# Kernel optimization log

Hardware: AMD Instinct MI355X
Metric: run time of the kernel (lower is better)

Reference implementation:

```python
import jax, jax.numpy as jnp
import numpy as np

B, S, D = 4, 2048, 1024


def setup_inputs() -> dict:
    key = jax.random.key(0)
    ks = jax.random.split(key, 7)
    s = 1.0 / np.sqrt(D)
    return {
        "x": jax.random.normal(ks[0], (B, S, D), dtype=jnp.float32),
        "Wq": jax.random.normal(ks[1], (D, D), dtype=jnp.float32) * s,
        "bq": jax.random.normal(ks[2], (D,), dtype=jnp.float32) * s,
        "Wk": jax.random.normal(ks[3], (D, D), dtype=jnp.float32) * s,
        "bk": jax.random.normal(ks[4], (D,), dtype=jnp.float32) * s,
        "Wv": jax.random.normal(ks[5], (D, D), dtype=jnp.float32) * s,
        "bv": jax.random.normal(ks[6], (D,), dtype=jnp.float32) * s,
    }


def reference(x, Wq, bq, Wk, bk, Wv, bv):
    # Linear layers: y = x @ W^T + b (torch nn.Linear convention)
    Q = jnp.einsum("bsd,ed->bse", x, Wq) + bq  # [B,S,D]
    K = jnp.einsum("bsd,ed->bse", x, Wk) + bk
    V = jnp.einsum("bsd,ed->bse", x, Wv) + bv
    d = x.shape[-1]
    scores = jnp.einsum("bqd,bkd->bqk", Q, K) / jnp.sqrt(jnp.float32(d))  # [B,S,S]
    weights = jax.nn.softmax(scores, axis=-1)
    O = jnp.einsum("bqk,bkd->bqd", weights, V)  # [B,S,D]
    return O
```

## Files before the change

kernel.cpp:

```cpp
#include <hip/hip_runtime.h>

typedef __bf16    bf16x8 __attribute__((ext_vector_type(8)));
typedef __bf16    bf16x4 __attribute__((ext_vector_type(4)));
typedef float     f32x4  __attribute__((ext_vector_type(4)));

#define BM 128
#define BN 128
#define BK 64

__device__ __forceinline__ void gload_lds16(const __bf16* g, __bf16* l) {
  __builtin_amdgcn_global_load_lds(
      (const __attribute__((address_space(1))) void*)g,
      (__attribute__((address_space(3))) void*)l,
      16, 0, 0);
}

__global__ void cvt_all(const float* __restrict__ x, const float* __restrict__ Wq,
                        const float* __restrict__ Wk, const float* __restrict__ Wv,
                        __bf16* __restrict__ xb, __bf16* __restrict__ Wqk,
                        __bf16* __restrict__ Wvb, float* __restrict__ lsum) {
  int b = blockIdx.x;
  if (b == 0) {
    for (int j = threadIdx.x; j < 8192; j += 256) lsum[j] = 0.f;
  }
  const float* src;
  __bf16* dst;
  int i;
  if (b < 8192) {
    src = x; dst = xb; i = b * 256 + threadIdx.x;
  } else {
    b -= 8192;
    const int mat = b >> 10;
    i = (b & 1023) * 256 + threadIdx.x;
    src = (mat == 0) ? Wq : (mat == 1) ? Wk : Wv;
    dst = (mat == 0) ? Wqk : (mat == 1) ? (Wqk + 1048576) : Wvb;
  }
  float4 v = ((const float4*)src)[i];
  bf16x4 o;
  o[0] = (__bf16)v.x; o[1] = (__bf16)v.y; o[2] = (__bf16)v.z; o[3] = (__bf16)v.w;
  ((bf16x4*)dst)[i] = o;
}

__device__ __forceinline__ void gemm_core(
    const __bf16* __restrict__ A, const __bf16* __restrict__ B,
    int lda, int ldb, int K, int bm0, int bn0,
    int tid, int wm, int wn, int quad, int l15,
    __bf16* As, __bf16* Bs, f32x4 (&acc)[4][4])
{
  const __bf16* Ag[4];
  const __bf16* Bg[4];
#pragma unroll
  for (int c = 0; c < 4; ++c) {
    const int r  = c * 32 + (tid >> 3);
    const int g  = (tid & 7) ^ (r & 7);
    Ag[c] = A + (size_t)(bm0 + r) * lda + g * 8;
    Bg[c] = B + (size_t)(bn0 + r) * ldb + g * 8;
  }

  for (int k0 = 0; k0 < K; k0 += BK) {
#pragma unroll
    for (int c = 0; c < 4; ++c) {
      gload_lds16(Ag[c] + k0, &As[c * 2048 + tid * 8]);
      gload_lds16(Bg[c] + k0, &Bs[c * 2048 + tid * 8]);
    }
    __syncthreads();

#pragma unroll
    for (int kk = 0; kk < 2; ++kk) {
      bf16x8 af[4], bfv[4];
#pragma unroll
      for (int i = 0; i < 4; ++i) {
        const int R = wm + i * 16 + l15;
        af[i] = *(const bf16x8*)&As[R * BK + (((kk * 4 + quad) ^ (R & 7)) * 8)];
      }
#pragma unroll
      for (int i = 0; i < 4; ++i) {
        const int R = wn + i * 16 + l15;
        bfv[i] = *(const bf16x8*)&Bs[R * BK + (((kk * 4 + quad) ^ (R & 7)) * 8)];
      }
#pragma unroll
      for (int mi = 0; mi < 4; ++mi)
#pragma unroll
        for (int ni = 0; ni < 4; ++ni)
          acc[mi][ni] = __builtin_amdgcn_mfma_f32_16x16x32_bf16(
              af[mi], bfv[ni], acc[mi][ni], 0, 0, 0);
    }
    __syncthreads();
  }
}

__global__ __launch_bounds__(256, 2)
void proj_qkv(const __bf16* __restrict__ xb, const __bf16* __restrict__ Wqk,
              const __bf16* __restrict__ Wvb,
              const float* __restrict__ bq, const float* __restrict__ bk,
              const float* __restrict__ bv,
              __bf16* __restrict__ Q, __bf16* __restrict__ Kb,
              __bf16* __restrict__ Vt)
{
  const int bid  = blockIdx.x;
  const int tid  = threadIdx.x;
  const int wave = tid >> 6;
  const int lane = tid & 63;
  const int quad = lane >> 4;
  const int l15  = lane & 15;
  const int wm   = (wave >> 1) * 64;
  const int wn   = (wave & 1) * 64;

  const bool isQK = bid < 1024;
  const __bf16* A;
  const __bf16* B;
  int bm0, bn0;
  if (isQK) {
    A = xb;  B = Wqk;
    bm0 = (bid & 63) * BM;  bn0 = (bid >> 6) * BN;
  } else {
    const int b2 = bid - 1024;
    A = Wvb; B = xb;
    bm0 = (b2 & 7) * BM;    bn0 = (b2 >> 3) * BN;
  }

  __shared__ __align__(16) __bf16 As[BM * BK];
  __shared__ __align__(16) __bf16 Bs[BN * BK];

  f32x4 acc[4][4];
#pragma unroll
  for (int i = 0; i < 4; ++i)
#pragma unroll
    for (int j = 0; j < 4; ++j)
      acc[i][j] = (f32x4){0.f, 0.f, 0.f, 0.f};

  gemm_core(A, B, 1024, 1024, 1024, bm0, bn0, tid, wm, wn, quad, l15,
            As, Bs, acc);

  if (isQK) {
#pragma unroll
    for (int mi = 0; mi < 4; ++mi) {
#pragma unroll
      for (int ni = 0; ni < 4; ++ni) {
        const int gn  = bn0 + wn + ni * 16 + l15;
        const int mat = gn >> 10;
        const int d   = gn & 1023;
        const float* bias = (mat == 0) ? bq : bk;
        __bf16* dst = (mat == 0) ? Q : Kb;
        const float bvv = bias[d];
#pragma unroll
        for (int r = 0; r < 4; ++r) {
          const int gm = bm0 + wm + mi * 16 + quad * 4 + r;
          dst[(size_t)gm * 1024 + d] = (__bf16)(acc[mi][ni][r] + bvv);
        }
      }
    }
  } else {
#pragma unroll
    for (int mi = 0; mi < 4; ++mi) {
#pragma unroll
      for (int ni = 0; ni < 4; ++ni) {
        const int gn = bn0 + wn + ni * 16 + l15;
        const int b  = gn >> 11, s = gn & 2047;
#pragma unroll
        for (int r = 0; r < 4; ++r) {
          const int gm = bm0 + wm + mi * 16 + quad * 4 + r;
          Vt[(size_t)b * (1024 * 2048) + (size_t)gm * 2048 + s] =
              (__bf16)(acc[mi][ni][r] + bv[gm]);
        }
      }
    }
  }
}

template<int MODE>
__global__ __launch_bounds__(256, 2)
void gemm_bt(const __bf16* __restrict__ A, const __bf16* __restrict__ B,
             float* __restrict__ C,
             int lda, int ldb, int ldc, int K,
             long sA, long sB, long sC,
             float* __restrict__ lsum,
             __bf16* __restrict__ out0)
{
  A += (long)blockIdx.z * sA;
  B += (long)blockIdx.z * sB;

  const int tid  = threadIdx.x;
  const int wave = tid >> 6;
  const int lane = tid & 63;
  const int quad = lane >> 4;
  const int l15  = lane & 15;
  const int bm0  = blockIdx.x * BM;
  const int bn0  = blockIdx.y * BN;
  const int wm   = (wave >> 1) * 64;
  const int wn   = (wave & 1) * 64;

  __shared__ __align__(16) __bf16 As[BM * BK];
  __shared__ __align__(16) __bf16 Bs[BN * BK];

  f32x4 acc[4][4];
#pragma unroll
  for (int i = 0; i < 4; ++i)
#pragma unroll
    for (int j = 0; j < 4; ++j)
      acc[i][j] = (f32x4){0.f, 0.f, 0.f, 0.f};

  gemm_core(A, B, lda, ldb, K, bm0, bn0, tid, wm, wn, quad, l15,
            As, Bs, acc);

  if (MODE == 2) {
#pragma unroll
    for (int mi = 0; mi < 4; ++mi) {
#pragma unroll
      for (int r = 0; r < 4; ++r) {
        const int gm = bm0 + wm + mi * 16 + quad * 4 + r;
        float part = 0.f;
#pragma unroll
        for (int ni = 0; ni < 4; ++ni) {
          const int gn = bn0 + wn + ni * 16 + l15;
          const __bf16 eb = (__bf16)__expf(acc[mi][ni][r] * 0.03125f);
          out0[(long)blockIdx.z * sC + (size_t)gm * ldc + gn] = eb;
          part += (float)eb;
        }
        part += __shfl_xor(part, 1);
        part += __shfl_xor(part, 2);
        part += __shfl_xor(part, 4);
        part += __shfl_xor(part, 8);
        if (l15 == 0)
          atomicAdd(&lsum[blockIdx.z * 2048 + gm], part);
      }
    }
  } else {
#pragma unroll
    for (int mi = 0; mi < 4; ++mi) {
#pragma unroll
      for (int r = 0; r < 4; ++r) {
        const int gm = bm0 + wm + mi * 16 + quad * 4 + r;
        const float rv = 1.0f / lsum[blockIdx.z * 2048 + gm];
#pragma unroll
        for (int ni = 0; ni < 4; ++ni) {
          const int gn = bn0 + wn + ni * 16 + l15;
          C[(long)blockIdx.z * sC + (size_t)gm * ldc + gn] = acc[mi][ni][r] * rv;
        }
      }
    }
  }
}

extern "C" void kernel_launch(void* const* d_in, const int* in_sizes, int n_in,
                              void* d_out, int out_size, void* d_ws, size_t ws_size,
                              hipStream_t stream) {
  const float* x  = (const float*)d_in[0];
  const float* Wq = (const float*)d_in[1];
  const float* bq = (const float*)d_in[2];
  const float* Wk = (const float*)d_in[3];
  const float* bk = (const float*)d_in[4];
  const float* Wv = (const float*)d_in[5];
  const float* bv = (const float*)d_in[6];
  float* out = (float*)d_out;

  char* ws = (char*)d_ws;
  __bf16* Q    = (__bf16*)(ws);
  __bf16* Kb   = (__bf16*)(ws + (16ull << 20));
  __bf16* Vt   = (__bf16*)(ws + (32ull << 20));
  __bf16* xb   = (__bf16*)(ws + (48ull << 20));
  __bf16* Wqk  = (__bf16*)(ws + (64ull << 20));
  __bf16* Wvb  = (__bf16*)(ws + (68ull << 20));
  __bf16* Sc   = (__bf16*)(ws + (48ull << 20));
  float*  lsum = (float*)(ws + (110ull << 20));

  dim3 blk(256);

  cvt_all<<<11264, blk, 0, stream>>>(x, Wq, Wk, Wv, xb, Wqk, Wvb, lsum);

  proj_qkv<<<1536, blk, 0, stream>>>(xb, Wqk, Wvb, bq, bk, bv, Q, Kb, Vt);

  gemm_bt<2><<<dim3(16, 16, 4), blk, 0, stream>>>(
      Q, Kb, nullptr, 1024, 1024, 2048, 1024,
      2048L * 1024, 2048L * 1024, 2048L * 2048,
      lsum, Sc);

  gemm_bt<3><<<dim3(16, 8, 4), blk, 0, stream>>>(
      Sc, Vt, out, 2048, 2048, 1024, 2048,
      2048L * 2048, 1024L * 2048, 2048L * 1024,
      lsum, nullptr);
}
```

Baseline: 245.0 us.

## Fuse all attention stages into one persistent kernel with grid barriers

Replaces the four separate launches (convert, QKV projection, scores+exp, PV) with one persistent kernel of 512 blocks that loops over tiles and separates stages with atomic-counter grid barriers. lsum and the barrier counter are zeroed by a memset. This removes per-launch overhead and inter-kernel gaps. In exchange it depends on all 512 blocks being co-resident to avoid deadlock, and the persistent tile loops may balance load less evenly than a full grid would (for example 1536 projection tiles over 512 blocks).

```diff
diff --git a/kernel.cpp b/kernel.cpp
--- a/kernel.cpp
+++ b/kernel.cpp
@@ -7,6 +7,7 @@
 #define BM 128
 #define BN 128
 #define BK 64
+#define NBLK 512
 
 __device__ __forceinline__ void gload_lds16(const __bf16* g, __bf16* l) {
   __builtin_amdgcn_global_load_lds(
@@ -15,34 +16,20 @@
       16, 0, 0);
 }
 
-__global__ void cvt_all(const float* __restrict__ x, const float* __restrict__ Wq,
-                        const float* __restrict__ Wk, const float* __restrict__ Wv,
-                        __bf16* __restrict__ xb, __bf16* __restrict__ Wqk,
-                        __bf16* __restrict__ Wvb, float* __restrict__ lsum) {
-  int b = blockIdx.x;
-  if (b == 0) {
-    for (int j = threadIdx.x; j < 8192; j += 256) lsum[j] = 0.f;
-  }
-  const float* src;
-  __bf16* dst;
-  int i;
-  if (b < 8192) {
-    src = x; dst = xb; i = b * 256 + threadIdx.x;
-  } else {
-    b -= 8192;
-    const int mat = b >> 10;
-    i = (b & 1023) * 256 + threadIdx.x;
-    src = (mat == 0) ? Wq : (mat == 1) ? Wk : Wv;
-    dst = (mat == 0) ? Wqk : (mat == 1) ? (Wqk + 1048576) : Wvb;
-  }
-  float4 v = ((const float4*)src)[i];
-  bf16x4 o;
-  o[0] = (__bf16)v.x; o[1] = (__bf16)v.y; o[2] = (__bf16)v.z; o[3] = (__bf16)v.w;
-  ((bf16x4*)dst)[i] = o;
+__device__ __forceinline__ void grid_barrier(unsigned* bar, unsigned target) {
+  __syncthreads();
+  if (threadIdx.x == 0) {
+    __threadfence();
+    atomicAdd(bar, 1u);
+    while (atomicAdd(bar, 0u) < target)
+      __builtin_amdgcn_s_sleep(2);
+    __threadfence();
+  }
+  __syncthreads();
 }
 
 __device__ __forceinline__ void gemm_core(
-    const __bf16* __restrict__ A, const __bf16* __restrict__ B,
+    const __bf16* A, const __bf16* B,
     int lda, int ldb, int K, int bm0, int bn0,
     int tid, int wm, int wn, int quad, int l15,
     __bf16* As, __bf16* Bs, f32x4 (&acc)[4][4])
@@ -90,14 +77,14 @@
 }
 
 __global__ __launch_bounds__(256, 2)
-void proj_qkv(const __bf16* __restrict__ xb, const __bf16* __restrict__ Wqk,
-              const __bf16* __restrict__ Wvb,
-              const float* __restrict__ bq, const float* __restrict__ bk,
-              const float* __restrict__ bv,
-              __bf16* __restrict__ Q, __bf16* __restrict__ Kb,
-              __bf16* __restrict__ Vt)
+void fused_attn(const float* __restrict__ x,  const float* __restrict__ Wq,
+                const float* __restrict__ bq, const float* __restrict__ Wk,
+                const float* __restrict__ bk, const float* __restrict__ Wv,
+                const float* __restrict__ bv, float* out,
+                __bf16* Q, __bf16* Kb, __bf16* Vt,
+                __bf16* xb, __bf16* Wqk, __bf16* Wvb,
+                __bf16* Sc, float* lsum, unsigned* bar)
 {
-  const int bid  = blockIdx.x;
   const int tid  = threadIdx.x;
   const int wave = tid >> 6;
   const int lane = tid & 63;
@@ -106,104 +93,110 @@
   const int wm   = (wave >> 1) * 64;
   const int wn   = (wave & 1) * 64;
 
-  const bool isQK = bid < 1024;
-  const __bf16* A;
-  const __bf16* B;
-  int bm0, bn0;
-  if (isQK) {
-    A = xb;  B = Wqk;
-    bm0 = (bid & 63) * BM;  bn0 = (bid >> 6) * BN;
-  } else {
-    const int b2 = bid - 1024;
-    A = Wvb; B = xb;
-    bm0 = (b2 & 7) * BM;    bn0 = (b2 >> 3) * BN;
-  }
-
   __shared__ __align__(16) __bf16 As[BM * BK];
   __shared__ __align__(16) __bf16 Bs[BN * BK];
 
-  f32x4 acc[4][4];
-#pragma unroll
-  for (int i = 0; i < 4; ++i)
-#pragma unroll
-    for (int j = 0; j < 4; ++j)
-      acc[i][j] = (f32x4){0.f, 0.f, 0.f, 0.f};
-
-  gemm_core(A, B, 1024, 1024, 1024, bm0, bn0, tid, wm, wn, quad, l15,
-            As, Bs, acc);
-
-  if (isQK) {
-#pragma unroll
-    for (int mi = 0; mi < 4; ++mi) {
-#pragma unroll
-      for (int ni = 0; ni < 4; ++ni) {
-        const int gn  = bn0 + wn + ni * 16 + l15;
-        const int mat = gn >> 10;
-        const int d   = gn & 1023;
-        const float* bias = (mat == 0) ? bq : bk;
-        __bf16* dst = (mat == 0) ? Q : Kb;
-        const float bvv = bias[d];
-#pragma unroll
-        for (int r = 0; r < 4; ++r) {
-          const int gm = bm0 + wm + mi * 16 + quad * 4 + r;
-          dst[(size_t)gm * 1024 + d] = (__bf16)(acc[mi][ni][r] + bvv);
-        }
-      }
-    }
-  } else {
-#pragma unroll
-    for (int mi = 0; mi < 4; ++mi) {
-#pragma unroll
-      for (int ni = 0; ni < 4; ++ni) {
-        const int gn = bn0 + wn + ni * 16 + l15;
-        const int b  = gn >> 11, s = gn & 2047;
-#pragma unroll
-        for (int r = 0; r < 4; ++r) {
-          const int gm = bm0 + wm + mi * 16 + quad * 4 + r;
-          Vt[(size_t)b * (1024 * 2048) + (size_t)gm * 2048 + s] =
-              (__bf16)(acc[mi][ni][r] + bv[gm]);
-        }
-      }
-    }
-  }
-}
-
-template<int MODE>
-__global__ __launch_bounds__(256, 2)
-void gemm_bt(const __bf16* __restrict__ A, const __bf16* __restrict__ B,
-             float* __restrict__ C,
-             int lda, int ldb, int ldc, int K,
-             long sA, long sB, long sC,
-             float* __restrict__ lsum,
-             __bf16* __restrict__ out0)
-{
-  A += (long)blockIdx.z * sA;
-  B += (long)blockIdx.z * sB;
-
-  const int tid  = threadIdx.x;
-  const int wave = tid >> 6;
-  const int lane = tid & 63;
-  const int quad = lane >> 4;
-  const int l15  = lane & 15;
-  const int bm0  = blockIdx.x * BM;
-  const int bn0  = blockIdx.y * BN;
-  const int wm   = (wave >> 1) * 64;
-  const int wn   = (wave & 1) * 64;
-
-  __shared__ __align__(16) __bf16 As[BM * BK];
-  __shared__ __align__(16) __bf16 Bs[BN * BK];
-
-  f32x4 acc[4][4];
-#pragma unroll
-  for (int i = 0; i < 4; ++i)
-#pragma unroll
-    for (int j = 0; j < 4; ++j)
-      acc[i][j] = (f32x4){0.f, 0.f, 0.f, 0.f};
-
-  gemm_core(A, B, lda, ldb, K, bm0, bn0, tid, wm, wn, quad, l15,
-            As, Bs, acc);
-
-  if (MODE == 2) {
+  {
+    const int g = blockIdx.x * 256 + tid;
+    const int gs = NBLK * 256;
+    for (int i = g; i < 2097152; i += gs) {
+      float4 v = ((const float4*)x)[i];
+      bf16x4 o;
+      o[0] = (__bf16)v.x; o[1] = (__bf16)v.y; o[2] = (__bf16)v.z; o[3] = (__bf16)v.w;
+      ((bf16x4*)xb)[i] = o;
+    }
+    for (int i = g; i < 786432; i += gs) {
+      const int mat = i >> 18;
+      const int j   = i & 262143;
+      const float* src = (mat == 0) ? Wq : (mat == 1) ? Wk : Wv;
+      __bf16* dst = (mat == 0) ? Wqk : (mat == 1) ? (Wqk + 1048576) : Wvb;
+      float4 v = ((const float4*)src)[j];
+      bf16x4 o;
+      o[0] = (__bf16)v.x; o[1] = (__bf16)v.y; o[2] = (__bf16)v.z; o[3] = (__bf16)v.w;
+      ((bf16x4*)dst)[j] = o;
+    }
+  }
+  grid_barrier(bar, NBLK);
+
+  for (int t = blockIdx.x; t < 1536; t += NBLK) {
+    const bool isQK = t < 1024;
+    const __bf16* A;
+    const __bf16* B;
+    int bm0, bn0;
+    if (isQK) {
+      A = xb;  B = Wqk;
+      bm0 = (t & 63) * BM;  bn0 = (t >> 6) * BN;
+    } else {
+      const int b2 = t - 1024;
+      A = Wvb; B = xb;
+      bm0 = (b2 & 7) * BM;  bn0 = (b2 >> 3) * BN;
+    }
+
+    f32x4 acc[4][4];
+#pragma unroll
+    for (int i = 0; i < 4; ++i)
+#pragma unroll
+      for (int j = 0; j < 4; ++j)
+        acc[i][j] = (f32x4){0.f, 0.f, 0.f, 0.f};
+
+    gemm_core(A, B, 1024, 1024, 1024, bm0, bn0, tid, wm, wn, quad, l15,
+              As, Bs, acc);
+
+    if (isQK) {
+#pragma unroll
+      for (int mi = 0; mi < 4; ++mi) {
+#pragma unroll
+        for (int ni = 0; ni < 4; ++ni) {
+          const int gn  = bn0 + wn + ni * 16 + l15;
+          const int mat = gn >> 10;
+          const int d   = gn & 1023;
+          const float* bias = (mat == 0) ? bq : bk;
+          __bf16* dst = (mat == 0) ? Q : Kb;
+          const float bvv = bias[d];
+#pragma unroll
+          for (int r = 0; r < 4; ++r) {
+            const int gm = bm0 + wm + mi * 16 + quad * 4 + r;
+            dst[(size_t)gm * 1024 + d] = (__bf16)(acc[mi][ni][r] + bvv);
+          }
+        }
+      }
+    } else {
+#pragma unroll
+      for (int mi = 0; mi < 4; ++mi) {
+#pragma unroll
+        for (int ni = 0; ni < 4; ++ni) {
+          const int gn = bn0 + wn + ni * 16 + l15;
+          const int b  = gn >> 11, s = gn & 2047;
+#pragma unroll
+          for (int r = 0; r < 4; ++r) {
+            const int gm = bm0 + wm + mi * 16 + quad * 4 + r;
+            Vt[(size_t)b * (1024 * 2048) + (size_t)gm * 2048 + s] =
+                (__bf16)(acc[mi][ni][r] + bv[gm]);
+          }
+        }
+      }
+    }
+  }
+  grid_barrier(bar, 2 * NBLK);
+
+  for (int t = blockIdx.x; t < 1024; t += NBLK) {
+    const int bm0 = (t & 15) * BM;
+    const int bn0 = ((t >> 4) & 15) * BN;
+    const int bz  = t >> 8;
+    const __bf16* A = Q  + (long)bz * (2048L * 1024);
+    const __bf16* B = Kb + (long)bz * (2048L * 1024);
+
+    f32x4 acc[4][4];
+#pragma unroll
+    for (int i = 0; i < 4; ++i)
+#pragma unroll
+      for (int j = 0; j < 4; ++j)
+        acc[i][j] = (f32x4){0.f, 0.f, 0.f, 0.f};
+
+    gemm_core(A, B, 1024, 1024, 1024, bm0, bn0, tid, wm, wn, quad, l15,
+              As, Bs, acc);
+
+    const long zc = (long)bz * (2048L * 2048);
 #pragma unroll
     for (int mi = 0; mi < 4; ++mi) {
 #pragma unroll
@@ -214,7 +207,7 @@
         for (int ni = 0; ni < 4; ++ni) {
           const int gn = bn0 + wn + ni * 16 + l15;
           const __bf16 eb = (__bf16)__expf(acc[mi][ni][r] * 0.03125f);
-          out0[(long)blockIdx.z * sC + (size_t)gm * ldc + gn] = eb;
+          Sc[zc + (size_t)gm * 2048 + gn] = eb;
           part += (float)eb;
         }
         part += __shfl_xor(part, 1);
@@ -222,20 +215,40 @@
         part += __shfl_xor(part, 4);
         part += __shfl_xor(part, 8);
         if (l15 == 0)
-          atomicAdd(&lsum[blockIdx.z * 2048 + gm], part);
-      }
-    }
-  } else {
+          atomicAdd(&lsum[bz * 2048 + gm], part);
+      }
+    }
+  }
+  grid_barrier(bar, 3 * NBLK);
+
+  for (int t = blockIdx.x; t < 512; t += NBLK) {
+    const int bm0 = (t & 15) * BM;
+    const int bn0 = ((t >> 4) & 7) * BN;
+    const int bz  = t >> 7;
+    const __bf16* A = Sc + (long)bz * (2048L * 2048);
+    const __bf16* B = Vt + (long)bz * (1024L * 2048);
+
+    f32x4 acc[4][4];
+#pragma unroll
+    for (int i = 0; i < 4; ++i)
+#pragma unroll
+      for (int j = 0; j < 4; ++j)
+        acc[i][j] = (f32x4){0.f, 0.f, 0.f, 0.f};
+
+    gemm_core(A, B, 2048, 2048, 2048, bm0, bn0, tid, wm, wn, quad, l15,
+              As, Bs, acc);
+
+    const long zc = (long)bz * (2048L * 1024);
 #pragma unroll
     for (int mi = 0; mi < 4; ++mi) {
 #pragma unroll
       for (int r = 0; r < 4; ++r) {
         const int gm = bm0 + wm + mi * 16 + quad * 4 + r;
-        const float rv = 1.0f / lsum[blockIdx.z * 2048 + gm];
+        const float rv = 1.0f / lsum[bz * 2048 + gm];
 #pragma unroll
         for (int ni = 0; ni < 4; ++ni) {
           const int gn = bn0 + wn + ni * 16 + l15;
-          C[(long)blockIdx.z * sC + (size_t)gm * ldc + gn] = acc[mi][ni][r] * rv;
+          out[zc + (size_t)gm * 1024 + gn] = acc[mi][ni][r] * rv;
         }
       }
     }
@@ -263,20 +276,11 @@
   __bf16* Wvb  = (__bf16*)(ws + (68ull << 20));
   __bf16* Sc   = (__bf16*)(ws + (48ull << 20));
   float*  lsum = (float*)(ws + (110ull << 20));
-
-  dim3 blk(256);
-
-  cvt_all<<<11264, blk, 0, stream>>>(x, Wq, Wk, Wv, xb, Wqk, Wvb, lsum);
-
-  proj_qkv<<<1536, blk, 0, stream>>>(xb, Wqk, Wvb, bq, bk, bv, Q, Kb, Vt);
-
-  gemm_bt<2><<<dim3(16, 16, 4), blk, 0, stream>>>(
-      Q, Kb, nullptr, 1024, 1024, 2048, 1024,
-      2048L * 1024, 2048L * 1024, 2048L * 2048,
-      lsum, Sc);
-
-  gemm_bt<3><<<dim3(16, 8, 4), blk, 0, stream>>>(
-      Sc, Vt, out, 2048, 2048, 1024, 2048,
-      2048L * 2048, 1024L * 2048, 2048L * 1024,
-      lsum, nullptr);
-}
+  unsigned* bar = (unsigned*)(ws + (110ull << 20) + 32768);
+
+  hipMemsetAsync(ws + (110ull << 20), 0, 32768 + 64, stream);
+
+  fused_attn<<<dim3(NBLK), dim3(256), 0, stream>>>(
+      x, Wq, bq, Wk, bk, Wv, bv, out,
+      Q, Kb, Vt, xb, Wqk, Wvb, Sc, lsum, bar);
+}
```

New measurement: 427.6 us. 74.5% more time.
